# Kernel tuning notes

Measured on AMD Instinct MI355X. Metric: run time of the kernel, lower is better.

## Reference

```python
import jax, jax.numpy as jnp
import numpy as np


def _spectral_normalize(W):
    # spectral_norm divides the weight by its largest singular value
    sigma = jnp.linalg.norm(W, ord=2)
    return W / sigma


def setup_inputs() -> dict:
    key = jax.random.key(0)
    ks = jax.random.split(key, 8)
    B, C, H, W = 2, 64, 96, 96
    C8 = C // 8
    x = jax.random.normal(ks[0], (B, C, H, W), dtype=jnp.float32)
    Wq = jax.random.normal(ks[1], (C8, C), dtype=jnp.float32) * 0.1
    bq = jax.random.normal(ks[2], (C8,), dtype=jnp.float32) * 0.1
    Wk = jax.random.normal(ks[3], (C8, C), dtype=jnp.float32) * 0.1
    bk = jax.random.normal(ks[4], (C8,), dtype=jnp.float32) * 0.1
    Wv = jax.random.normal(ks[5], (C, C), dtype=jnp.float32) * 0.1
    bv = jax.random.normal(ks[6], (C,), dtype=jnp.float32) * 0.1
    gamma = jnp.ones((1,), dtype=jnp.float32)
    return {"x": x, "Wq": Wq, "bq": bq, "Wk": Wk, "bk": bk,
            "Wv": Wv, "bv": bv, "gamma": gamma}


def reference(x, Wq, bq, Wk, bk, Wv, bv, gamma):
    B, C, H, W = x.shape
    xf = x.reshape(B, C, H * W)                       # [B, C, N]
    Wq_n = _spectral_normalize(Wq)
    Wk_n = _spectral_normalize(Wk)
    Wv_n = _spectral_normalize(Wv)
    # 1x1 Conv1d == matmul over channel dim
    f = jnp.einsum('oc,bcn->bon', Wq_n, xf) + bq[None, :, None]   # [B, C/8, N]
    g = jnp.einsum('oc,bcn->bon', Wk_n, xf) + bk[None, :, None]   # [B, C/8, N]
    h = jnp.einsum('oc,bcn->bon', Wv_n, xf) + bv[None, :, None]   # [B, C, N]
    # scores[b,i,j] = sum_c f[b,c,i] * g[b,c,j];  softmax over dim=1 (i)
    scores = jnp.einsum('bci,bcj->bij', f, g)                      # [B, N, N]
    beta = jax.nn.softmax(scores, axis=1)
    # o[b,c,j] = sum_i h[b,c,i] * beta[b,i,j]
    o = gamma[0] * jnp.einsum('bci,bij->bcj', h, beta) + xf
    return o.reshape(B, C, H, W)
```

## Files before the change

kernel.cpp:

```cpp
#include <hip/hip_runtime.h>


#define N_PIX 9216
#define N_B   2
#define N_C   64

typedef _Float16 half8  __attribute__((ext_vector_type(8)));
typedef _Float16 half4v __attribute__((ext_vector_type(4)));
typedef float    float4v __attribute__((ext_vector_type(4)));
typedef int      int4v  __attribute__((ext_vector_type(4)));

#define LOG2E 1.44269504088896340736f
#define EXP_SHIFT 12.0f

__global__ __launch_bounds__(64) void k_sigma(const float* __restrict__ Wq,
                                              const float* __restrict__ Wk,
                                              const float* __restrict__ Wv,
                                              float* __restrict__ sig,
                                              unsigned* __restrict__ maxKu) {
  __shared__ float G8[8][8];
  __shared__ float Wl[64 * 64];
  __shared__ _Float16 Wh[64 * 80];
  __shared__ _Float16 Gh[64 * 80];
  const int t = threadIdx.x;
  const int mat = blockIdx.x;
  if (mat == 0 && t < 2) maxKu[t] = 0u;
  if (mat < 2) {
    const float* W = (mat == 0) ? Wq : Wk;
    const int i = t >> 3, j = t & 7;
    float g = 0.f;
    for (int c = 0; c < 64; ++c) g += W[i * 64 + c] * W[j * 64 + c];
    G8[i][j] = g;
    __syncthreads();
    const int L = t & 7;
    float G0[8], Gr[8];
    for (int k = 0; k < 8; ++k) { G0[k] = G8[L][k]; Gr[k] = G0[k]; }
    for (int it = 0; it < 8; ++it) {
      float g2[8] = {0, 0, 0, 0, 0, 0, 0, 0};
      for (int k = 0; k < 8; ++k) {
        float gik = Gr[k];
        for (int jj = 0; jj < 8; ++jj) g2[jj] += gik * __shfl(Gr[jj], k, 64);
      }
      float mx = 0.f;
      for (int jj = 0; jj < 8; ++jj) mx = fmaxf(mx, fabsf(g2[jj]));
      for (int d = 1; d < 8; d <<= 1) mx = fmaxf(mx, __shfl_xor(mx, d, 64));
      float r = 1.f / mx;
      for (int jj = 0; jj < 8; ++jj) Gr[jj] = g2[jj] * r;
    }
    float u = 0.f;
    for (int jj = 0; jj < 8; ++jj) u += Gr[jj];
    float y = 0.f;
    for (int k = 0; k < 8; ++k) y += G0[k] * __shfl(u, k, 64);
    float nu = u * y, de = u * u;
    for (int d = 1; d < 8; d <<= 1) { nu += __shfl_xor(nu, d, 64); de += __shfl_xor(de, d, 64); }
    if (t == 0) sig[mat] = sqrtf(nu / de);
  } else {
    for (int idx = t; idx < 4096; idx += 64) Wl[idx] = Wv[idx];
    __syncthreads();
    for (int idx = t; idx < 4096; idx += 64) Wh[(idx >> 6) * 80 + (idx & 63)] = (_Float16)Wl[idx];
    __syncthreads();
    const int lane15 = t & 15, quad = t >> 4;
    half8 fr[4][2];
    for (int rb = 0; rb < 4; ++rb)
      for (int kc = 0; kc < 2; ++kc)
        fr[rb][kc] = *(const half8*)&Wh[(lane15 + 16 * rb) * 80 + 32 * kc + 8 * quad];
    float4v D[4][4];
    for (int mb = 0; mb < 4; ++mb) for (int nb = 0; nb < 4; ++nb) D[mb][nb] = (float4v){0.f, 0.f, 0.f, 0.f};
    for (int kc = 0; kc < 2; ++kc)
      for (int mb = 0; mb < 4; ++mb)
        for (int nb = 0; nb < 4; ++nb)
          D[mb][nb] = __builtin_amdgcn_mfma_f32_16x16x32_f16(fr[mb][kc], fr[nb][kc], D[mb][nb], 0, 0, 0);
    for (int it = 0; it < 8; ++it) {
      float mx = 0.f;
      for (int mb = 0; mb < 4; ++mb) for (int nb = 0; nb < 4; ++nb) for (int r = 0; r < 4; ++r)
        mx = fmaxf(mx, fabsf(D[mb][nb][r]));
      for (int d = 1; d < 64; d <<= 1) mx = fmaxf(mx, __shfl_xor(mx, d, 64));
      float rs = 1.f / mx;
      for (int mb = 0; mb < 4; ++mb) for (int nb = 0; nb < 4; ++nb) for (int r = 0; r < 4; ++r)
        Gh[(4 * quad + r + 16 * mb) * 80 + lane15 + 16 * nb] = (_Float16)(D[mb][nb][r] * rs);
      __syncthreads();
      if (it == 7) break;
      for (int rb = 0; rb < 4; ++rb)
        for (int kc = 0; kc < 2; ++kc)
          fr[rb][kc] = *(const half8*)&Gh[(lane15 + 16 * rb) * 80 + 32 * kc + 8 * quad];
      for (int mb = 0; mb < 4; ++mb) for (int nb = 0; nb < 4; ++nb) D[mb][nb] = (float4v){0.f, 0.f, 0.f, 0.f};
      for (int kc = 0; kc < 2; ++kc)
        for (int mb = 0; mb < 4; ++mb)
          for (int nb = 0; nb < 4; ++nb)
            D[mb][nb] = __builtin_amdgcn_mfma_f32_16x16x32_f16(fr[mb][kc], fr[nb][kc], D[mb][nb], 0, 0, 0);
      __syncthreads();
    }
    float u = 0.f;
    for (int c = 0; c < 64; ++c) u += (float)Gh[t * 80 + c];
    float z = 0.f;
    for (int i2 = 0; i2 < 64; ++i2) z += Wl[i2 * 64 + t] * __shfl(u, i2, 64);
    float nu = z * z, de = u * u;
    for (int d = 1; d < 64; d <<= 1) { nu += __shfl_xor(nu, d, 64); de += __shfl_xor(de, d, 64); }
    if (t == 0) sig[2] = sqrtf(nu / de);
  }
}

__global__ __launch_bounds__(256) void k_fgh(const float* __restrict__ x,
                                             const float* __restrict__ Wq, const float* __restrict__ bq,
                                             const float* __restrict__ Wk, const float* __restrict__ bk,
                                             const float* __restrict__ Wv, const float* __restrict__ bv,
                                             const float* __restrict__ sig,
                                             _Float16* __restrict__ K16,
                                             _Float16* __restrict__ Q16,
                                             _Float16* __restrict__ VT16,
                                             unsigned* __restrict__ maxKu) {
  __shared__ _Float16 Wsh[80 * 64];
  __shared__ float bsh[80];
  const int t = threadIdx.x;
  const float iq = LOG2E / sig[0], ik = 1.0f / sig[1], iv = 1.0f / sig[2];
  for (int idx = t; idx < 80 * 64; idx += 256) {
    const int m = idx >> 6, c = idx & 63;
    float v;
    if (m < 8)       v = Wq[m * 64 + c] * iq;
    else if (m < 16) v = Wk[(m - 8) * 64 + c] * ik;
    else             v = Wv[(m - 16) * 64 + c] * iv;
    Wsh[idx] = (_Float16)v;
  }
  if (t < 80) {
    float v;
    if (t < 8)       v = bq[t] * LOG2E;
    else if (t < 16) v = bk[t - 8];
    else             v = bv[t - 16];
    bsh[t] = v;
  }
  __syncthreads();
  const int wave = t >> 6;
  const int lane = t & 63;
  const int lane15 = lane & 15, quad = lane >> 4;
  const int tile = blockIdx.x * 4 + wave;
  const int b = tile / 576;
  const int n = (tile % 576) * 16 + lane15;
  half8 wf[5][2];
  for (int mb = 0; mb < 5; ++mb)
    for (int kc = 0; kc < 2; ++kc)
      wf[mb][kc] = *(const half8*)&Wsh[(lane15 + 16 * mb) * 64 + 32 * kc + 8 * quad];
  float4v acc[5];
  for (int mb = 0; mb < 5; ++mb) acc[mb] = *(const float4v*)&bsh[16 * mb + 4 * quad];
  const float* xb = x + (size_t)b * N_C * N_PIX;
  for (int kc = 0; kc < 2; ++kc) {
    half8 bf;
    for (int j = 0; j < 8; ++j)
      bf[j] = (_Float16)xb[(size_t)(32 * kc + 8 * quad + j) * N_PIX + n];
    for (int mb = 0; mb < 5; ++mb)
      acc[mb] = __builtin_amdgcn_mfma_f32_16x16x32_f16(wf[mb][kc], bf, acc[mb], 0, 0, 0);
  }
  {
    _Float16* dstK = K16 + ((size_t)b * N_PIX + n) * 8;
    _Float16* dstQ = Q16 + ((size_t)b * N_PIX + n) * 8;
    for (int r = 0; r < 4; ++r) {
      const int m = 4 * quad + r;
      const _Float16 v = (_Float16)acc[0][r];
      if (m < 8) dstK[m] = v; else dstQ[m - 8] = v;
    }
  }
  for (int mb = 1; mb < 5; ++mb)
    for (int r = 0; r < 4; ++r) {
      const int c = 4 * quad + r + 16 * (mb - 1);
      VT16[((size_t)b * N_C + c) * N_PIX + n] = (_Float16)acc[mb][r];
    }
  float sq = 0.f;
  if (quad < 2)
    for (int r = 0; r < 4; ++r) sq += acc[0][r] * acc[0][r];
  sq += __shfl_xor(sq, 16, 64);
  for (int d = 1; d < 64; d <<= 1) sq = fmaxf(sq, __shfl_xor(sq, d, 64));
  if (lane == 0) atomicMax(&maxKu[b], __float_as_uint(sq));
}


__device__ __forceinline__ void gload16(const _Float16* g, _Float16* l) {
  __builtin_amdgcn_global_load_lds(
      (const __attribute__((address_space(1))) void*)g,
      (__attribute__((address_space(3))) void*)l, 16, 0, 0);
}

#define VMWAIT5() asm volatile("s_waitcnt vmcnt(5)" ::: "memory")
#define DS2(D0, D1, P0, P1)                                              \
  asm volatile("ds_read_b128 %0, %2\n\t"                                 \
               "ds_read_b128 %1, %3\n\t"                                 \
               "s_waitcnt lgkmcnt(0)"                                    \
               : "=&v"(D0), "=&v"(D1) : "v"(P0), "v"(P1) : "memory")
#define DS4(D0, D1, D2, D3, P0, P1, P2, P3)                              \
  asm volatile("ds_read_b128 %0, %4\n\t"                                 \
               "ds_read_b128 %1, %5\n\t"                                 \
               "ds_read_b128 %2, %6\n\t"                                 \
               "ds_read_b128 %3, %7\n\t"                                 \
               "s_waitcnt lgkmcnt(0)"                                    \
               : "=&v"(D0), "=&v"(D1), "=&v"(D2), "=&v"(D3)              \
               : "v"(P0), "v"(P1), "v"(P2), "v"(P3) : "memory")
typedef const __attribute__((address_space(3))) _Float16* lds_cp;

__global__ __launch_bounds__(256, 3) void k_attn(const _Float16* __restrict__ K16,
                                                 const _Float16* __restrict__ Q16,
                                                 const _Float16* __restrict__ VT16,
                                                 const unsigned* __restrict__ maxKu,
                                                 const float* __restrict__ x,
                                                 const float* __restrict__ gamma,
                                                 float* __restrict__ out) {
  __shared__ __align__(16) _Float16 SM[4][6400];
  const int wave = threadIdx.x >> 6;
  const int lane = threadIdx.x & 63;
  const int lane15 = lane & 15, quad = lane >> 4;
  const int tile = blockIdx.x;
  const int b = tile / 288;
  const int jb = (tile % 288) * 32;
  const float gm = gamma[0];
  const _Float16* Kb = K16 + (size_t)b * N_PIX * 8;
  const _Float16* Vb = VT16 + (size_t)b * N_C * N_PIX;
  _Float16* Rg = SM[wave];
  _Float16* Pl = Rg + 5120;
  const int cl = lane >> 2, kk = lane & 3;
  const int gsw = (kk ^ ((cl >> 1) & 3)) * 8;
  const int ksrc = lane & 31;
  const int vslot = (quad ^ ((lane15 >> 1) & 3)) * 8;

  half8 qf0 = {}, qf1 = {};
  if (quad == 0) {
    qf0 = *(const half8*)(Q16 + ((size_t)b * N_PIX + jb + lane15) * 8);
    qf1 = *(const half8*)(Q16 + ((size_t)b * N_PIX + jb + 16 + lane15) * 8);
  }
  const float maxK = sqrtf(__uint_as_float(maxKu[b]));
  float nq0 = 0.f, nq1 = 0.f;
  if (quad == 0)
#pragma unroll
    for (int j = 0; j < 8; ++j) {
      nq0 += (float)qf0[j] * (float)qf0[j];
      nq1 += (float)qf1[j] * (float)qf1[j];
    }
  nq0 = __shfl(nq0, lane15, 64);
  nq1 = __shfl(nq1, lane15, 64);
  const float M0 = sqrtf(nq0) * maxK - EXP_SHIFT;
  const float M1 = sqrtf(nq1) * maxK - EXP_SHIFT;

  float4v a00 = {0.f,0.f,0.f,0.f}, a01 = {0.f,0.f,0.f,0.f}, a02 = {0.f,0.f,0.f,0.f}, a03 = {0.f,0.f,0.f,0.f};
  float4v a10 = {0.f,0.f,0.f,0.f}, a11 = {0.f,0.f,0.f,0.f}, a12 = {0.f,0.f,0.f,0.f}, a13 = {0.f,0.f,0.f,0.f};
  float ls0 = 0.f, ls1 = 0.f;
  const float4v f4z = {0.f, 0.f, 0.f, 0.f};

#define STAGE(SLOT, I0)                                                          \
  {                                                                              \
    const int _i = (I0);                                                         \
    gload16(Kb + (size_t)(_i + ksrc) * 8, Rg + 4096 + (SLOT) * 512);             \
    gload16(Vb + (size_t)cl * N_PIX + _i + gsw,        Rg + (SLOT) * 2048);      \
    gload16(Vb + (size_t)(16 + cl) * N_PIX + _i + gsw, Rg + (SLOT) * 2048 + 512);\
    gload16(Vb + (size_t)(32 + cl) * N_PIX + _i + gsw, Rg + (SLOT) * 2048 + 1024);\
    gload16(Vb + (size_t)(48 + cl) * N_PIX + _i + gsw, Rg + (SLOT) * 2048 + 1536);\
  }

  STAGE(0, 32 * wave)

#pragma unroll 1
  for (int r = 0; r < 72; ++r) {
    const int slot = r & 1, nslot = slot ^ 1;
    const int i1 = (r < 71) ? (128 * (r + 1) + 32 * wave) : (128 * 71 + 32 * wave);
    STAGE(nslot, i1)
    VMWAIT5();
    int4v k0i, k1i;
    {
      lds_cp pk0 = (lds_cp)(Rg + 4096 + slot * 512 + lane15 * 8);
      lds_cp pk1 = (lds_cp)(Rg + 4096 + slot * 512 + 128 + lane15 * 8);
      DS2(k0i, k1i, pk0, pk1);
    }
    const half8 kf0 = __builtin_bit_cast(half8, k0i);
    const half8 kf1 = __builtin_bit_cast(half8, k1i);
    float4v s00 = __builtin_amdgcn_mfma_f32_16x16x32_f16(kf0, qf0, f4z, 0, 0, 0);
    float4v s10 = __builtin_amdgcn_mfma_f32_16x16x32_f16(kf1, qf0, f4z, 0, 0, 0);
    float4v s01 = __builtin_amdgcn_mfma_f32_16x16x32_f16(kf0, qf1, f4z, 0, 0, 0);
    float4v s11 = __builtin_amdgcn_mfma_f32_16x16x32_f16(kf1, qf1, f4z, 0, 0, 0);
    half4v h00, h10, h01, h11;
#pragma unroll
    for (int rr = 0; rr < 4; ++rr) {
      const float p00 = __builtin_amdgcn_exp2f(s00[rr] - M0);
      const float p10 = __builtin_amdgcn_exp2f(s10[rr] - M0);
      const float p01 = __builtin_amdgcn_exp2f(s01[rr] - M1);
      const float p11 = __builtin_amdgcn_exp2f(s11[rr] - M1);
      h00[rr] = (_Float16)p00; ls0 += (float)h00[rr];
      h10[rr] = (_Float16)p10; ls0 += (float)h10[rr];
      h01[rr] = (_Float16)p01; ls1 += (float)h01[rr];
      h11[rr] = (_Float16)p11; ls1 += (float)h11[rr];
    }
    *(half4v*)&Pl[lane15 * 40 + 4 * quad] = h00;
    *(half4v*)&Pl[lane15 * 40 + 16 + 4 * quad] = h10;
    *(half4v*)&Pl[(16 + lane15) * 40 + 4 * quad] = h01;
    *(half4v*)&Pl[(16 + lane15) * 40 + 16 + 4 * quad] = h11;
    const half8 pf0 = *(const half8*)&Pl[lane15 * 40 + 8 * quad];
    const half8 pf1 = *(const half8*)&Pl[(16 + lane15) * 40 + 8 * quad];
    int4v v0i, v1i, v2i, v3i;
    {
      lds_cp pv0 = (lds_cp)(Rg + slot * 2048 + lane15 * 32 + vslot);
      lds_cp pv1 = (lds_cp)(Rg + slot * 2048 + 512 + lane15 * 32 + vslot);
      lds_cp pv2 = (lds_cp)(Rg + slot * 2048 + 1024 + lane15 * 32 + vslot);
      lds_cp pv3 = (lds_cp)(Rg + slot * 2048 + 1536 + lane15 * 32 + vslot);
      DS4(v0i, v1i, v2i, v3i, pv0, pv1, pv2, pv3);
    }
    a00 = __builtin_amdgcn_mfma_f32_16x16x32_f16(pf0, __builtin_bit_cast(half8, v0i), a00, 0, 0, 0);
    a01 = __builtin_amdgcn_mfma_f32_16x16x32_f16(pf0, __builtin_bit_cast(half8, v1i), a01, 0, 0, 0);
    a02 = __builtin_amdgcn_mfma_f32_16x16x32_f16(pf0, __builtin_bit_cast(half8, v2i), a02, 0, 0, 0);
    a03 = __builtin_amdgcn_mfma_f32_16x16x32_f16(pf0, __builtin_bit_cast(half8, v3i), a03, 0, 0, 0);
    a10 = __builtin_amdgcn_mfma_f32_16x16x32_f16(pf1, __builtin_bit_cast(half8, v0i), a10, 0, 0, 0);
    a11 = __builtin_amdgcn_mfma_f32_16x16x32_f16(pf1, __builtin_bit_cast(half8, v1i), a11, 0, 0, 0);
    a12 = __builtin_amdgcn_mfma_f32_16x16x32_f16(pf1, __builtin_bit_cast(half8, v2i), a12, 0, 0, 0);
    a13 = __builtin_amdgcn_mfma_f32_16x16x32_f16(pf1, __builtin_bit_cast(half8, v3i), a13, 0, 0, 0);
  }
#undef STAGE
  asm volatile("s_waitcnt vmcnt(0)" ::: "memory");

  float* Ow = (float*)Rg;
  float* Lw = (float*)Rg + 1088;
  ls0 += __shfl_xor(ls0, 16, 64); ls0 += __shfl_xor(ls0, 32, 64);
  ls1 += __shfl_xor(ls1, 16, 64); ls1 += __shfl_xor(ls1, 32, 64);
  if (quad == 0) { Lw[lane15] = ls0; Lw[16 + lane15] = ls1; }
#pragma unroll
  for (int rr = 0; rr < 4; ++rr) {
    Ow[lane * 17 + rr]      = a00[rr];
    Ow[lane * 17 + 4 + rr]  = a01[rr];
    Ow[lane * 17 + 8 + rr]  = a02[rr];
    Ow[lane * 17 + 12 + rr] = a03[rr];
  }
  __syncthreads();
  float4v lt0 = {0.f, 0.f, 0.f, 0.f}, lt1 = {0.f, 0.f, 0.f, 0.f};
#pragma unroll
  for (int w = 0; w < 4; ++w) {
    const float* Lww = (const float*)SM[w] + 1088;
#pragma unroll
    for (int rr = 0; rr < 4; ++rr) {
      lt0[rr] += Lww[4 * quad + rr];
      lt1[rr] += Lww[16 + 4 * quad + rr];
    }
  }
  const int ch = 16 * wave + lane15;
  const float* xb = x + (size_t)b * N_C * N_PIX;
  float* ob = out + (size_t)b * N_C * N_PIX;
  {
    float4v osum = {0.f, 0.f, 0.f, 0.f};
#pragma unroll
    for (int w = 0; w < 4; ++w) {
      const float* Oww = (const float*)SM[w];
#pragma unroll
      for (int rr = 0; rr < 4; ++rr) osum[rr] += Oww[lane * 17 + 4 * wave + rr];
    }
    const size_t idx = (size_t)ch * N_PIX + jb + 4 * quad;
    const float4v xr = *(const float4v*)(xb + idx);
    float4v o;
#pragma unroll
    for (int rr = 0; rr < 4; ++rr) o[rr] = gm * osum[rr] / lt0[rr] + xr[rr];
    *(float4v*)(ob + idx) = o;
  }
  __syncthreads();
#pragma unroll
  for (int rr = 0; rr < 4; ++rr) {
    Ow[lane * 17 + rr]      = a10[rr];
    Ow[lane * 17 + 4 + rr]  = a11[rr];
    Ow[lane * 17 + 8 + rr]  = a12[rr];
    Ow[lane * 17 + 12 + rr] = a13[rr];
  }
  __syncthreads();
  {
    float4v osum = {0.f, 0.f, 0.f, 0.f};
#pragma unroll
    for (int w = 0; w < 4; ++w) {
      const float* Oww = (const float*)SM[w];
#pragma unroll
      for (int rr = 0; rr < 4; ++rr) osum[rr] += Oww[lane * 17 + 4 * wave + rr];
    }
    const size_t idx = (size_t)ch * N_PIX + jb + 16 + 4 * quad;
    const float4v xr = *(const float4v*)(xb + idx);
    float4v o;
#pragma unroll
    for (int rr = 0; rr < 4; ++rr) o[rr] = gm * osum[rr] / lt1[rr] + xr[rr];
    *(float4v*)(ob + idx) = o;
  }
}

extern "C" void kernel_launch(void* const* d_in, const int* in_sizes, int n_in,
                              void* d_out, int out_size, void* d_ws, size_t ws_size,
                              hipStream_t stream) {
  const float* x     = (const float*)d_in[0];
  const float* Wq    = (const float*)d_in[1];
  const float* bq    = (const float*)d_in[2];
  const float* Wk    = (const float*)d_in[3];
  const float* bk    = (const float*)d_in[4];
  const float* Wv    = (const float*)d_in[5];
  const float* bv    = (const float*)d_in[6];
  const float* gamma = (const float*)d_in[7];
  float* out = (float*)d_out;

  char* ws = (char*)d_ws;
  float*    sig   = (float*)ws;
  unsigned* maxKu = (unsigned*)(ws + 16);
  _Float16* K16   = (_Float16*)(ws + 10752);
  _Float16* Q16   = (_Float16*)(ws + 10752 + 294912);
  _Float16* VT16  = (_Float16*)(ws + 10752 + 2 * 294912);

  hipLaunchKernelGGL(k_sigma, dim3(3), dim3(64), 0, stream, Wq, Wk, Wv, sig, maxKu);
  hipLaunchKernelGGL(k_fgh, dim3(288), dim3(256), 0, stream,
                     x, Wq, bq, Wk, bk, Wv, bv, sig, K16, Q16, VT16, maxKu);
  hipLaunchKernelGGL(k_attn, dim3(576), dim3(256), 0, stream, K16, Q16, VT16, maxKu, x, gamma, out);
}
```

Baseline: 178.1 us.

## Switch attention inner loop to 32x32x16 MFMA with register-shuffled P operand

Replaces the 16x16x32 MFMA tiling in the attention loop with 32x32x16 MFMAs. The max-shift subtraction is folded into the score MFMA's accumulator init, and the probability tile is rearranged into the B operand with cross-half lane shuffles instead of an LDS round trip. Inline-asm LDS reads are replaced by plain loads, the V swizzle changes to match the new read pattern, and the epilogue writes scalar per-pixel outputs. This removes the per-iteration P staging through shared memory and the LDS scratch space for it. In exchange, half of the K operand lanes are zeroed, so part of the score MFMA's reduction depth is wasted. The output stores also become strided scalar accesses.

New measurement: 175.0 us. No clear change (-1.8%).

```diff
diff --git a/kernel.cpp b/kernel.cpp
--- a/kernel.cpp
+++ b/kernel.cpp
@@ -6,8 +6,9 @@
 #define N_C   64
 
 typedef _Float16 half8  __attribute__((ext_vector_type(8)));
-typedef _Float16 half4v __attribute__((ext_vector_type(4)));
+typedef _Float16 half2v __attribute__((ext_vector_type(2)));
 typedef float    float4v __attribute__((ext_vector_type(4)));
+typedef float    float16v __attribute__((ext_vector_type(16)));
 typedef int      int4v  __attribute__((ext_vector_type(4)));
 
 #define LOG2E 1.44269504088896340736f
@@ -177,22 +178,7 @@
       (const __attribute__((address_space(1))) void*)g,
       (__attribute__((address_space(3))) void*)l, 16, 0, 0);
 }
-
 #define VMWAIT5() asm volatile("s_waitcnt vmcnt(5)" ::: "memory")
-#define DS2(D0, D1, P0, P1)                                              \
-  asm volatile("ds_read_b128 %0, %2\n\t"                                 \
-               "ds_read_b128 %1, %3\n\t"                                 \
-               "s_waitcnt lgkmcnt(0)"                                    \
-               : "=&v"(D0), "=&v"(D1) : "v"(P0), "v"(P1) : "memory")
-#define DS4(D0, D1, D2, D3, P0, P1, P2, P3)                              \
-  asm volatile("ds_read_b128 %0, %4\n\t"                                 \
-               "ds_read_b128 %1, %5\n\t"                                 \
-               "ds_read_b128 %2, %6\n\t"                                 \
-               "ds_read_b128 %3, %7\n\t"                                 \
-               "s_waitcnt lgkmcnt(0)"                                    \
-               : "=&v"(D0), "=&v"(D1), "=&v"(D2), "=&v"(D3)              \
-               : "v"(P0), "v"(P1), "v"(P2), "v"(P3) : "memory")
-typedef const __attribute__((address_space(3))) _Float16* lds_cp;
 
 __global__ __launch_bounds__(256, 3) void k_attn(const _Float16* __restrict__ K16,
                                                  const _Float16* __restrict__ Q16,
@@ -201,10 +187,10 @@
                                                  const float* __restrict__ x,
                                                  const float* __restrict__ gamma,
                                                  float* __restrict__ out) {
-  __shared__ __align__(16) _Float16 SM[4][6400];
+  __shared__ __align__(16) _Float16 SM[4][5120];
   const int wave = threadIdx.x >> 6;
   const int lane = threadIdx.x & 63;
-  const int lane15 = lane & 15, quad = lane >> 4;
+  const int q31 = lane & 31, hi = lane >> 5;
   const int tile = blockIdx.x;
   const int b = tile / 288;
   const int jb = (tile % 288) * 32;
@@ -212,39 +198,33 @@
   const _Float16* Kb = K16 + (size_t)b * N_PIX * 8;
   const _Float16* Vb = VT16 + (size_t)b * N_C * N_PIX;
   _Float16* Rg = SM[wave];
-  _Float16* Pl = Rg + 5120;
   const int cl = lane >> 2, kk = lane & 3;
-  const int gsw = (kk ^ ((cl >> 1) & 3)) * 8;
-  const int ksrc = lane & 31;
-  const int vslot = (quad ^ ((lane15 >> 1) & 3)) * 8;
-
-  half8 qf0 = {}, qf1 = {};
-  if (quad == 0) {
-    qf0 = *(const half8*)(Q16 + ((size_t)b * N_PIX + jb + lane15) * 8);
-    qf1 = *(const half8*)(Q16 + ((size_t)b * N_PIX + jb + 16 + lane15) * 8);
-  }
+  const int gsw = (kk ^ (cl & 3)) * 8;
+  const int vq = q31 * 32;
+  const int voff00 = vq + (((0 + hi) ^ (q31 & 3)) << 3);
+  const int voff01 = vq + (((2 + hi) ^ (q31 & 3)) << 3);
+  const int voff10 = 1024 + voff00;
+  const int voff11 = 1024 + voff01;
+
+  half8 qf = {};
+  if (hi == 0) qf = *(const half8*)(Q16 + ((size_t)b * N_PIX + jb + q31) * 8);
   const float maxK = sqrtf(__uint_as_float(maxKu[b]));
-  float nq0 = 0.f, nq1 = 0.f;
-  if (quad == 0)
-#pragma unroll
-    for (int j = 0; j < 8; ++j) {
-      nq0 += (float)qf0[j] * (float)qf0[j];
-      nq1 += (float)qf1[j] * (float)qf1[j];
-    }
-  nq0 = __shfl(nq0, lane15, 64);
-  nq1 = __shfl(nq1, lane15, 64);
-  const float M0 = sqrtf(nq0) * maxK - EXP_SHIFT;
-  const float M1 = sqrtf(nq1) * maxK - EXP_SHIFT;
-
-  float4v a00 = {0.f,0.f,0.f,0.f}, a01 = {0.f,0.f,0.f,0.f}, a02 = {0.f,0.f,0.f,0.f}, a03 = {0.f,0.f,0.f,0.f};
-  float4v a10 = {0.f,0.f,0.f,0.f}, a11 = {0.f,0.f,0.f,0.f}, a12 = {0.f,0.f,0.f,0.f}, a13 = {0.f,0.f,0.f,0.f};
-  float ls0 = 0.f, ls1 = 0.f;
-  const float4v f4z = {0.f, 0.f, 0.f, 0.f};
+  float nq = 0.f;
+#pragma unroll
+  for (int j = 0; j < 8; ++j) nq += (float)qf[j] * (float)qf[j];
+  nq += __shfl_xor(nq, 32, 64);
+  const float M = sqrtf(nq) * maxK - EXP_SHIFT;
+  float16v sinit;
+#pragma unroll
+  for (int r2 = 0; r2 < 16; ++r2) sinit[r2] = -M;
+
+  float16v acc0 = {}, acc1 = {};
+  float ls = 0.f;
 
 #define STAGE(SLOT, I0)                                                          \
   {                                                                              \
     const int _i = (I0);                                                         \
-    gload16(Kb + (size_t)(_i + ksrc) * 8, Rg + 4096 + (SLOT) * 512);             \
+    gload16(Kb + (size_t)(_i + q31) * 8, Rg + 4096 + (SLOT) * 512);              \
     gload16(Vb + (size_t)cl * N_PIX + _i + gsw,        Rg + (SLOT) * 2048);      \
     gload16(Vb + (size_t)(16 + cl) * N_PIX + _i + gsw, Rg + (SLOT) * 2048 + 512);\
     gload16(Vb + (size_t)(32 + cl) * N_PIX + _i + gsw, Rg + (SLOT) * 2048 + 1024);\
@@ -259,120 +239,79 @@
     const int i1 = (r < 71) ? (128 * (r + 1) + 32 * wave) : (128 * 71 + 32 * wave);
     STAGE(nslot, i1)
     VMWAIT5();
-    int4v k0i, k1i;
-    {
-      lds_cp pk0 = (lds_cp)(Rg + 4096 + slot * 512 + lane15 * 8);
-      lds_cp pk1 = (lds_cp)(Rg + 4096 + slot * 512 + 128 + lane15 * 8);
-      DS2(k0i, k1i, pk0, pk1);
-    }
-    const half8 kf0 = __builtin_bit_cast(half8, k0i);
-    const half8 kf1 = __builtin_bit_cast(half8, k1i);
-    float4v s00 = __builtin_amdgcn_mfma_f32_16x16x32_f16(kf0, qf0, f4z, 0, 0, 0);
-    float4v s10 = __builtin_amdgcn_mfma_f32_16x16x32_f16(kf1, qf0, f4z, 0, 0, 0);
-    float4v s01 = __builtin_amdgcn_mfma_f32_16x16x32_f16(kf0, qf1, f4z, 0, 0, 0);
-    float4v s11 = __builtin_amdgcn_mfma_f32_16x16x32_f16(kf1, qf1, f4z, 0, 0, 0);
-    half4v h00, h10, h01, h11;
-#pragma unroll
-    for (int rr = 0; rr < 4; ++rr) {
-      const float p00 = __builtin_amdgcn_exp2f(s00[rr] - M0);
-      const float p10 = __builtin_amdgcn_exp2f(s10[rr] - M0);
-      const float p01 = __builtin_amdgcn_exp2f(s01[rr] - M1);
-      const float p11 = __builtin_amdgcn_exp2f(s11[rr] - M1);
-      h00[rr] = (_Float16)p00; ls0 += (float)h00[rr];
-      h10[rr] = (_Float16)p10; ls0 += (float)h10[rr];
-      h01[rr] = (_Float16)p01; ls1 += (float)h01[rr];
-      h11[rr] = (_Float16)p11; ls1 += (float)h11[rr];
-    }
-    *(half4v*)&Pl[lane15 * 40 + 4 * quad] = h00;
-    *(half4v*)&Pl[lane15 * 40 + 16 + 4 * quad] = h10;
-    *(half4v*)&Pl[(16 + lane15) * 40 + 4 * quad] = h01;
-    *(half4v*)&Pl[(16 + lane15) * 40 + 16 + 4 * quad] = h11;
-    const half8 pf0 = *(const half8*)&Pl[lane15 * 40 + 8 * quad];
-    const half8 pf1 = *(const half8*)&Pl[(16 + lane15) * 40 + 8 * quad];
-    int4v v0i, v1i, v2i, v3i;
-    {
-      lds_cp pv0 = (lds_cp)(Rg + slot * 2048 + lane15 * 32 + vslot);
-      lds_cp pv1 = (lds_cp)(Rg + slot * 2048 + 512 + lane15 * 32 + vslot);
-      lds_cp pv2 = (lds_cp)(Rg + slot * 2048 + 1024 + lane15 * 32 + vslot);
-      lds_cp pv3 = (lds_cp)(Rg + slot * 2048 + 1536 + lane15 * 32 + vslot);
-      DS4(v0i, v1i, v2i, v3i, pv0, pv1, pv2, pv3);
-    }
-    a00 = __builtin_amdgcn_mfma_f32_16x16x32_f16(pf0, __builtin_bit_cast(half8, v0i), a00, 0, 0, 0);
-    a01 = __builtin_amdgcn_mfma_f32_16x16x32_f16(pf0, __builtin_bit_cast(half8, v1i), a01, 0, 0, 0);
-    a02 = __builtin_amdgcn_mfma_f32_16x16x32_f16(pf0, __builtin_bit_cast(half8, v2i), a02, 0, 0, 0);
-    a03 = __builtin_amdgcn_mfma_f32_16x16x32_f16(pf0, __builtin_bit_cast(half8, v3i), a03, 0, 0, 0);
-    a10 = __builtin_amdgcn_mfma_f32_16x16x32_f16(pf1, __builtin_bit_cast(half8, v0i), a10, 0, 0, 0);
-    a11 = __builtin_amdgcn_mfma_f32_16x16x32_f16(pf1, __builtin_bit_cast(half8, v1i), a11, 0, 0, 0);
-    a12 = __builtin_amdgcn_mfma_f32_16x16x32_f16(pf1, __builtin_bit_cast(half8, v2i), a12, 0, 0, 0);
-    a13 = __builtin_amdgcn_mfma_f32_16x16x32_f16(pf1, __builtin_bit_cast(half8, v3i), a13, 0, 0, 0);
+    half8 kf = *(const half8*)&Rg[4096 + slot * 512 + q31 * 8];
+    if (hi) kf = (half8){};
+    float16v s = __builtin_amdgcn_mfma_f32_32x32x16_f16(kf, qf, sinit, 0, 0, 0);
+    int pk[8];
+#pragma unroll
+    for (int u = 0; u < 8; ++u) {
+      const float p0 = __builtin_amdgcn_exp2f(s[2 * u]);
+      const float p1 = __builtin_amdgcn_exp2f(s[2 * u + 1]);
+      ls += p0 + p1;
+      pk[u] = __builtin_bit_cast(int, __builtin_amdgcn_cvt_pkrtz(p0, p1));
+    }
+    const int t0 = hi ? pk[0] : pk[2];
+    const int t1 = hi ? pk[1] : pk[3];
+    const int t2 = hi ? pk[4] : pk[6];
+    const int t3 = hi ? pk[5] : pk[7];
+    const int x0 = __shfl_xor(t0, 32, 64);
+    const int x1 = __shfl_xor(t1, 32, 64);
+    const int x2 = __shfl_xor(t2, 32, 64);
+    const int x3 = __shfl_xor(t3, 32, 64);
+    int4v B0i, B1i;
+    B0i[0] = hi ? x0 : pk[0];  B0i[1] = hi ? x1 : pk[1];
+    B0i[2] = hi ? pk[2] : x0;  B0i[3] = hi ? pk[3] : x1;
+    B1i[0] = hi ? x2 : pk[4];  B1i[1] = hi ? x3 : pk[5];
+    B1i[2] = hi ? pk[6] : x2;  B1i[3] = hi ? pk[7] : x3;
+    const half8 P0 = __builtin_bit_cast(half8, B0i);
+    const half8 P1 = __builtin_bit_cast(half8, B1i);
+    const _Float16* Vs = Rg + slot * 2048;
+    const half8 v00 = *(const half8*)&Vs[voff00];
+    const half8 v01 = *(const half8*)&Vs[voff01];
+    const half8 v10 = *(const half8*)&Vs[voff10];
+    const half8 v11 = *(const half8*)&Vs[voff11];
+    acc0 = __builtin_amdgcn_mfma_f32_32x32x16_f16(v00, P0, acc0, 0, 0, 0);
+    acc0 = __builtin_amdgcn_mfma_f32_32x32x16_f16(v01, P1, acc0, 0, 0, 0);
+    acc1 = __builtin_amdgcn_mfma_f32_32x32x16_f16(v10, P0, acc1, 0, 0, 0);
+    acc1 = __builtin_amdgcn_mfma_f32_32x32x16_f16(v11, P1, acc1, 0, 0, 0);
   }
 #undef STAGE
   asm volatile("s_waitcnt vmcnt(0)" ::: "memory");
 
   float* Ow = (float*)Rg;
-  float* Lw = (float*)Rg + 1088;
-  ls0 += __shfl_xor(ls0, 16, 64); ls0 += __shfl_xor(ls0, 32, 64);
-  ls1 += __shfl_xor(ls1, 16, 64); ls1 += __shfl_xor(ls1, 32, 64);
-  if (quad == 0) { Lw[lane15] = ls0; Lw[16 + lane15] = ls1; }
-#pragma unroll
-  for (int rr = 0; rr < 4; ++rr) {
-    Ow[lane * 17 + rr]      = a00[rr];
-    Ow[lane * 17 + 4 + rr]  = a01[rr];
-    Ow[lane * 17 + 8 + rr]  = a02[rr];
-    Ow[lane * 17 + 12 + rr] = a03[rr];
-  }
+  float* Lw = (float*)Rg + 1100;
+  ls += __shfl_xor(ls, 32, 64);
+  if (hi == 0) Lw[q31] = ls;
+#pragma unroll
+  for (int r2 = 0; r2 < 16; ++r2) Ow[lane * 17 + r2] = acc0[r2];
   __syncthreads();
-  float4v lt0 = {0.f, 0.f, 0.f, 0.f}, lt1 = {0.f, 0.f, 0.f, 0.f};
-#pragma unroll
-  for (int w = 0; w < 4; ++w) {
-    const float* Lww = (const float*)SM[w] + 1088;
-#pragma unroll
-    for (int rr = 0; rr < 4; ++rr) {
-      lt0[rr] += Lww[4 * quad + rr];
-      lt1[rr] += Lww[16 + 4 * quad + rr];
-    }
-  }
-  const int ch = 16 * wave + lane15;
+  float ltot = 0.f;
+#pragma unroll
+  for (int w = 0; w < 4; ++w) ltot += ((const float*)SM[w])[1100 + q31];
+  const float inv = gm / ltot;
   const float* xb = x + (size_t)b * N_C * N_PIX;
   float* ob = out + (size_t)b * N_C * N_PIX;
-  {
-    float4v osum = {0.f, 0.f, 0.f, 0.f};
-#pragma unroll
-    for (int w = 0; w < 4; ++w) {
-      const float* Oww = (const float*)SM[w];
-#pragma unroll
-      for (int rr = 0; rr < 4; ++rr) osum[rr] += Oww[lane * 17 + 4 * wave + rr];
-    }
-    const size_t idx = (size_t)ch * N_PIX + jb + 4 * quad;
-    const float4v xr = *(const float4v*)(xb + idx);
-    float4v o;
-#pragma unroll
-    for (int rr = 0; rr < 4; ++rr) o[rr] = gm * osum[rr] / lt0[rr] + xr[rr];
-    *(float4v*)(ob + idx) = o;
+#pragma unroll
+  for (int r2 = 0; r2 < 16; ++r2) {
+    float osum = 0.f;
+#pragma unroll
+    for (int w = 0; w < 4; ++w) osum += ((const float*)SM[w])[lane * 17 + r2];
+    const int c = (r2 & 3) + 8 * (r2 >> 2) + 4 * hi;
+    const size_t idx = (size_t)c * N_PIX + jb + q31;
+    ob[idx] = osum * inv + xb[idx];
   }
   __syncthreads();
 #pragma unroll
-  for (int rr = 0; rr < 4; ++rr) {
-    Ow[lane * 17 + rr]      = a10[rr];
-    Ow[lane * 17 + 4 + rr]  = a11[rr];
-    Ow[lane * 17 + 8 + rr]  = a12[rr];
-    Ow[lane * 17 + 12 + rr] = a13[rr];
-  }
+  for (int r2 = 0; r2 < 16; ++r2) Ow[lane * 17 + r2] = acc1[r2];
   __syncthreads();
-  {
-    float4v osum = {0.f, 0.f, 0.f, 0.f};
-#pragma unroll
-    for (int w = 0; w < 4; ++w) {
-      const float* Oww = (const float*)SM[w];
-#pragma unroll
-      for (int rr = 0; rr < 4; ++rr) osum[rr] += Oww[lane * 17 + 4 * wave + rr];
-    }
-    const size_t idx = (size_t)ch * N_PIX + jb + 16 + 4 * quad;
-    const float4v xr = *(const float4v*)(xb + idx);
-    float4v o;
-#pragma unroll
-    for (int rr = 0; rr < 4; ++rr) o[rr] = gm * osum[rr] / lt1[rr] + xr[rr];
-    *(float4v*)(ob + idx) = o;
+#pragma unroll
+  for (int r2 = 0; r2 < 16; ++r2) {
+    float osum = 0.f;
+#pragma unroll
+    for (int w = 0; w < 4; ++w) osum += ((const float*)SM[w])[lane * 17 + r2];
+    const int c = 32 + (r2 & 3) + 8 * (r2 >> 2) + 4 * hi;
+    const size_t idx = (size_t)c * N_PIX + jb + q31;
+    ob[idx] = osum * inv + xb[idx];
   }
 }
 
```
